# Kernel optimization log

Measured on AMD Instinct MI355X. Metric: run time of the kernel, lower is better.

Reference implementation:

```python
import jax, jax.numpy as jnp
import numpy as np

C = 192   # channels (class attr)
N = 196   # tokens per stream; 2N = 392, R feat dim = 784
B = 256

def _pw(x, w, b):
    # 1x1 Conv1d == pointwise channel mix: x [B,Ci,L] -> [B,Co,L]
    return jnp.einsum('oi,bil->bol', w, x) + b[None, :, None]

def _bn(x, g, beta, m, v):
    # eval-mode BatchNorm1d
    inv = g / jnp.sqrt(v + 1e-5)
    return (x - m[None, :, None]) * inv[None, :, None] + beta[None, :, None]

def setup_inputs():
    key = jax.random.key(0)
    ks = jax.random.split(key, 24)
    s = 1.0 / np.sqrt(C)
    d = {}
    d['x'] = jax.random.normal(ks[0], (B, N, C), dtype=jnp.float32)
    d['y'] = jax.random.normal(ks[1], (B, N, C), dtype=jnp.float32)
    # linear_conv_1: Conv1d(C,C,1) + BN + ReLU
    d['w1'] = jax.random.normal(ks[2], (C, C), dtype=jnp.float32) * s
    d['b1'] = jax.random.normal(ks[3], (C,), dtype=jnp.float32) * 0.01
    d['g1'] = jnp.ones((C,), jnp.float32)
    d['be1'] = jnp.zeros((C,), jnp.float32)
    d['m1'] = jax.random.normal(ks[4], (C,), dtype=jnp.float32) * 0.1
    d['v1'] = jax.random.uniform(ks[5], (C,), dtype=jnp.float32) + 0.5
    # linear_conv_2
    d['w2'] = jax.random.normal(ks[6], (C, C), dtype=jnp.float32) * s
    d['b2'] = jax.random.normal(ks[7], (C,), dtype=jnp.float32) * 0.01
    d['g2'] = jnp.ones((C,), jnp.float32)
    d['be2'] = jnp.zeros((C,), jnp.float32)
    d['m2'] = jax.random.normal(ks[8], (C,), dtype=jnp.float32) * 0.1
    d['v2'] = jax.random.uniform(ks[9], (C,), dtype=jnp.float32) + 0.5
    # linear_conv_3: Conv1d(C,C,1)
    d['w3'] = jax.random.normal(ks[10], (C, C), dtype=jnp.float32) * s
    d['b3'] = jax.random.normal(ks[11], (C,), dtype=jnp.float32) * 0.01
    # linear_conv_4: Conv1d(784,784,1)
    d['w4'] = jax.random.normal(ks[12], (784, 784), dtype=jnp.float32) / np.sqrt(784)
    d['b4'] = jax.random.normal(ks[13], (784,), dtype=jnp.float32) * 0.01
    # linear_conv_5: Conv1d(C+784,1,1)
    d['w5'] = jax.random.normal(ks[14], (1, C + 784), dtype=jnp.float32) / np.sqrt(C + 784)
    d['b5'] = jax.random.normal(ks[15], (1,), dtype=jnp.float32) * 0.01
    return d

def reference(x, y, w1, b1, g1, be1, m1, v1, w2, b2, g2, be2, m2, v2, w3, b3, w4, b4, w5, b5):
    xp = jnp.swapaxes(x, 1, 2)  # [B,C,N]
    yp = jnp.swapaxes(y, 1, 2)
    phi_x = jax.nn.relu(_bn(_pw(xp, w1, b1), g1, be1, m1, v1))
    phi_y = jax.nn.relu(_bn(_pw(yp, w2, b2), g2, be2, m2, v2))
    cat_phi = jnp.concatenate([phi_x, phi_y], axis=2)            # [B,C,2N]
    A = jnp.einsum('bcn,bcm->bnm', cat_phi, cat_phi)             # [B,2N,2N]
    # R[b,i,:] = cat(A[b,i,:], A[b,:,i]) for i in 0..2N-1, then permute(0,2,1)
    R = jnp.concatenate([A, jnp.swapaxes(A, 1, 2)], axis=2)      # [B,2N,4N]
    R = jnp.swapaxes(R, 1, 2)                                    # [B,4N,2N] = [B,784,392]
    v = _pw(cat_phi, w3, b3)                                     # [B,C,392]
    v_ = _pw(R, w4, b4)                                          # [B,784,392]
    cat_v = jnp.concatenate([v, v_], axis=1)                     # [B,976,392]
    W = _pw(cat_v, w5, b5)                                       # [B,1,392]
    out = xp * W[:, :, :N] + yp * W[:, :, N:]                    # [B,C,N]
    return out
```

## Files before the change

### kernel.cpp

```cpp
#include <hip/hip_runtime.h>
#include <hip/hip_bf16.h>

typedef __attribute__((ext_vector_type(8))) short bf16x8;
typedef __attribute__((ext_vector_type(4))) float f32x4;

#define CDIM 192
#define NTOK 196
#define LTOT 392
#define BDIM 256
#define NBE 64

__device__ __forceinline__ ushort f2bf(float f) {
  uint u = __float_as_uint(f);
  u = (u + 0x7FFFu + ((u >> 16) & 1u)) >> 16;
  return (ushort)u;
}
__device__ __forceinline__ float bf2f(ushort h) {
  return __uint_as_float(((uint)h) << 16);
}
__device__ __forceinline__ uint pk2(float lo, float hi) {
  __hip_bfloat162 t = __float22bfloat162_rn(float2{lo, hi});
  uint r;
  __builtin_memcpy(&r, &t, 4);
  return r;
}
__device__ __forceinline__ float wave_reduce(float a) {
#pragma unroll
  for (int off = 32; off > 0; off >>= 1) a += __shfl_xor(a, off);
  return a;
}

__global__ __launch_bounds__(256) void prep_kernel(
    const float* __restrict__ w1, const float* __restrict__ b1, const float* __restrict__ g1,
    const float* __restrict__ be1, const float* __restrict__ m1, const float* __restrict__ v1,
    const float* __restrict__ w2, const float* __restrict__ b2, const float* __restrict__ g2,
    const float* __restrict__ be2, const float* __restrict__ m2, const float* __restrict__ v2,
    const float* __restrict__ w3, const float* __restrict__ b3,
    const float* __restrict__ w4, const float* __restrict__ b4,
    const float* __restrict__ w5, const float* __restrict__ b5,
    ushort* __restrict__ w1b, ushort* __restrict__ w2b,
    float* __restrict__ u3, float* __restrict__ u4, float* __restrict__ cvecs,
    float* __restrict__ Kc, float* __restrict__ s) {
  const int bid = blockIdx.x;
  const int wid = threadIdx.x >> 6, lane = threadIdx.x & 63;
  if (bid < NBE) {
    for (int i = bid * BDIM + threadIdx.x; i < 123264; i += NBE * BDIM) {
      if (i < 36864) {
        int o = i / CDIM;
        float inv = g1[o] * rsqrtf(v1[o] + 1e-5f);
        w1b[i] = f2bf(w1[i] * inv);
      } else if (i < 73728) {
        int j = i - 36864; int o = j / CDIM;
        float inv = g2[o] * rsqrtf(v2[o] + 1e-5f);
        w2b[j] = f2bf(w2[j] * inv);
      } else if (i < 74112) {
        int k = i - 73728; int h = k / CDIM, o = k % CDIM;
        const float* bb = h ? b2 : b1; const float* gg = h ? g2 : g1;
        const float* bee = h ? be2 : be1;
        const float* mm = h ? m2 : m1; const float* vv = h ? v2 : v1;
        float inv = gg[o] * rsqrtf(vv[o] + 1e-5f);
        cvecs[k] = (bb[o] - mm[o]) * inv + bee[o];
      } else {
        s[i - 74112] = 0.f;
      }
    }
  } else if (bid < NBE + 48) {
    int j = (bid - NBE) * 4 + wid;
    float a = 0.f;
    for (int c = lane; c < CDIM; c += 64) a += w5[c] * w3[c * CDIM + j];
    a = wave_reduce(a);
    if (lane == 0) u3[j] = a;
  } else if (bid < NBE + 48 + 98) {
    int j = (bid - NBE - 48) * 4 + wid;
    float a = 0.f;
    for (int o = lane; o < 784; o += 64)
      a += w5[CDIM + o] * (w4[o * 784 + j] + w4[o * 784 + j + LTOT]);
    a = wave_reduce(a);
    if (lane == 0) u4[j] = a;
  } else {
    if (wid == 0) {
      float a = 0.f;
      for (int i = lane; i < CDIM + 784; i += 64)
        a += (i < CDIM) ? w5[i] * b3[i] : w5[i] * b4[i - CDIM];
      a = wave_reduce(a);
      if (lane == 0) Kc[0] = a + b5[0];
    }
  }
}

__global__ __launch_bounds__(256) void phi_kernel(
    const float* __restrict__ x, const float* __restrict__ y,
    const ushort* __restrict__ w1b, const ushort* __restrict__ w2b,
    const float* __restrict__ cvecs, const float* __restrict__ u4,
    ushort* __restrict__ phiT, float* __restrict__ s) {
  const int bh = blockIdx.x, b = bh >> 1, h = bh & 1;
  const float* __restrict__ src = (h ? y : x) + (size_t)b * NTOK * CDIM;
  const ushort* __restrict__ wb = h ? w2b : w1b;
  __shared__ ushort Abuf[2][32 * CDIM];
  __shared__ ushort Obuf[32 * CDIM];
  __shared__ float u4s[224];
  __shared__ float cs[CDIM];
  const int tid = threadIdx.x;
  for (int i = tid; i < 224; i += BDIM) u4s[i] = (i < NTOK) ? u4[h * NTOK + i] : 0.f;
  for (int i = tid; i < CDIM; i += BDIM) cs[i] = cvecs[h * CDIM + i];

  const int wid = tid >> 6, lane = tid & 63;
  const int lrow = lane & 15, kgrp = lane >> 4;
  const int cbase = wid * 48 + lrow;

  bf16x8 bfr[3][6];
#pragma unroll
  for (int ct = 0; ct < 3; ct++)
#pragma unroll
    for (int kk = 0; kk < 6; kk++)
      bfr[ct][kk] = *(const bf16x8*)(wb + (size_t)(cbase + ct * 16) * CDIM + kk * 32 + kgrp * 8);
  __syncthreads();
  const float csr[3] = {cs[cbase], cs[cbase + 16], cs[cbase + 32]};

  const float4* src4 = (const float4*)src;
  const int NF4 = NTOK * CDIM / 4;
  float sp[3] = {0.f, 0.f, 0.f};

  float4 pf[6];
#pragma unroll
  for (int p = 0; p < 6; p++) {
    pf[p] = src4[p * 256 + tid];
  }

  for (int r = 0; r < 7; r++) {
    ushort* Ab = &Abuf[r & 1][0];
#pragma unroll
    for (int p = 0; p < 6; p++) {
      const int fi = r * 1536 + p * 256 + tid;
      const int rowg = fi / 48;
      const int col = (fi - rowg * 48) * 4;
      const int rl = rowg & 31;
      uint2 wv;
      if (fi < NF4) { wv.x = pk2(pf[p].x, pf[p].y); wv.y = pk2(pf[p].z, pf[p].w); }
      else          { wv.x = 0u; wv.y = 0u; }
      uint addr = (uint)(rl * (CDIM * 2) + col * 2);
      addr ^= (uint)((rl & 7) << 4);
      *(uint2*)((char*)Ab + addr) = wv;
    }
    if (r < 6) {
#pragma unroll
      for (int p = 0; p < 6; p++) {
        const int fi = (r + 1) * 1536 + p * 256 + tid;
        pf[p] = (fi < NF4) ? src4[fi] : float4{0.f, 0.f, 0.f, 0.f};
      }
    }
    __syncthreads();
#pragma unroll
    for (int tt = 0; tt < 2; tt++) {
      bf16x8 afr[6];
#pragma unroll
      for (int kk = 0; kk < 6; kk++) {
        uint addr = (uint)((tt * 16 + lrow) * (CDIM * 2) + (kk * 32 + kgrp * 8) * 2);
        addr ^= (uint)((lrow & 7) << 4);
        afr[kk] = *(const bf16x8*)((const char*)Ab + addr);
      }
      f32x4 acc0 = {0.f,0.f,0.f,0.f}, acc1 = {0.f,0.f,0.f,0.f}, acc2 = {0.f,0.f,0.f,0.f};
#pragma unroll
      for (int kk = 0; kk < 6; kk++) {
        acc0 = __builtin_amdgcn_mfma_f32_16x16x32_bf16(afr[kk], bfr[0][kk], acc0, 0, 0, 0);
        acc1 = __builtin_amdgcn_mfma_f32_16x16x32_bf16(afr[kk], bfr[1][kk], acc1, 0, 0, 0);
        acc2 = __builtin_amdgcn_mfma_f32_16x16x32_bf16(afr[kk], bfr[2][kk], acc2, 0, 0, 0);
      }
      const int ll = tt * 16 + 4 * kgrp;
      const float4 u4v = *(const float4*)&u4s[r * 32 + ll];
      auto epi = [&](const f32x4& acc, int ct, float& spc) {
        const float v0 = fmaxf(acc[0] + csr[ct], 0.f);
        const float v1 = fmaxf(acc[1] + csr[ct], 0.f);
        const float v2 = fmaxf(acc[2] + csr[ct], 0.f);
        const float v3 = fmaxf(acc[3] + csr[ct], 0.f);
        const uint p01 = pk2(v0, v1), p23 = pk2(v2, v3);
        const int c = cbase + ct * 16;
#pragma unroll
        for (int j = 0; j < 4; j++) {
          const int row = ll + j;
          uint addr = (uint)(row * (CDIM * 2) + c * 2);
          addr ^= (uint)((row & 7) << 4);
          const uint piece = (j == 0) ? (p01 & 0xFFFFu) : (j == 1) ? (p01 >> 16)
                           : (j == 2) ? (p23 & 0xFFFFu) : (p23 >> 16);
          *(ushort*)((char*)Obuf + addr) = (ushort)piece;
        }
        spc += u4v.x * v0 + u4v.y * v1 + u4v.z * v2 + u4v.w * v3;
      };
      epi(acc0, 0, sp[0]); epi(acc1, 1, sp[1]); epi(acc2, 2, sp[2]);
    }
    __syncthreads();
    const int rows = min(32, NTOK - r * 32);
    const int nel = rows * CDIM;
    ushort* dst = phiT + ((size_t)b * LTOT + h * NTOK + r * 32) * CDIM;
    for (int off = tid * 8; off < nel; off += BDIM * 8) {
      const int row = off / CDIM;
      uint addr = (uint)(off * 2) ^ (uint)((row & 7) << 4);
      uint4 v = *(const uint4*)((const char*)Obuf + addr);
      *(uint4*)(dst + off) = v;
    }
  }
#pragma unroll
  for (int ct = 0; ct < 3; ct++) {
    float v = sp[ct];
    v += __shfl_xor(v, 16);
    v += __shfl_xor(v, 32);
    if (kgrp == 0) atomicAdd(&s[b * CDIM + cbase + ct * 16], v);
  }
}

__global__ __launch_bounds__(256) void wout_kernel(
    const float* __restrict__ x, const float* __restrict__ y,
    const ushort* __restrict__ phiT, const float* __restrict__ s,
    const float* __restrict__ u3, const float* __restrict__ Kc,
    float* __restrict__ out) {
  const int bid = blockIdx.x;
  const int b = bid / 7, nt = bid % 7;
  const int n0 = nt * 28;
  __shared__ float coeff[CDIM];
  __shared__ float Wl[56];
  __shared__ float tile[28][193];
  const int tid = threadIdx.x;
  for (int i = tid; i < CDIM; i += BDIM) coeff[i] = u3[i] + s[b * CDIM + i];
  __syncthreads();
  const int wv = tid >> 6, lane = tid & 63;
  const int rloc = wv * 16 + (lane >> 2), g4 = lane & 3;
  if (rloc < 56) {
    const int lg = (rloc < 28) ? (n0 + rloc) : (NTOK + n0 + rloc - 28);
    const ushort* p = phiT + ((size_t)b * LTOT + lg) * CDIM + g4 * 48;
    float acc = 0.f;
#pragma unroll
    for (int q = 0; q < 12; q++) {
      ushort4 v = *(const ushort4*)(p + q * 4);
      const float* cf = &coeff[g4 * 48 + q * 4];
      acc += cf[0] * bf2f(v.x) + cf[1] * bf2f(v.y) +
             cf[2] * bf2f(v.z) + cf[3] * bf2f(v.w);
    }
    acc += __shfl_xor(acc, 1);
    acc += __shfl_xor(acc, 2);
    if (g4 == 0) Wl[rloc] = acc + Kc[0];
  }
  __syncthreads();
  for (int i = tid; i < 28 * 48; i += BDIM) {
    const int nl = i / 48, c4 = (i % 48) * 4;
    const size_t xi = ((size_t)b * NTOK + n0 + nl) * CDIM + c4;
    const float4 xv = *(const float4*)&x[xi];
    const float4 yv = *(const float4*)&y[xi];
    const float wx = Wl[nl], wy = Wl[28 + nl];
    tile[nl][c4 + 0] = xv.x * wx + yv.x * wy;
    tile[nl][c4 + 1] = xv.y * wx + yv.y * wy;
    tile[nl][c4 + 2] = xv.z * wx + yv.z * wy;
    tile[nl][c4 + 3] = xv.w * wx + yv.w * wy;
  }
  __syncthreads();
  for (int i = tid; i < CDIM * 7; i += BDIM) {
    const int c = i / 7, nq = i % 7;
    float4 o;
    o.x = tile[nq * 4 + 0][c]; o.y = tile[nq * 4 + 1][c];
    o.z = tile[nq * 4 + 2][c]; o.w = tile[nq * 4 + 3][c];
    *(float4*)&out[((size_t)b * CDIM + c) * NTOK + n0 + nq * 4] = o;
  }
}

extern "C" void kernel_launch(void* const* d_in, const int* in_sizes, int n_in,
                              void* d_out, int out_size, void* d_ws, size_t ws_size,
                              hipStream_t stream) {
  const float* x   = (const float*)d_in[0];
  const float* y   = (const float*)d_in[1];
  const float* w1  = (const float*)d_in[2];
  const float* b1  = (const float*)d_in[3];
  const float* g1  = (const float*)d_in[4];
  const float* be1 = (const float*)d_in[5];
  const float* m1  = (const float*)d_in[6];
  const float* v1  = (const float*)d_in[7];
  const float* w2  = (const float*)d_in[8];
  const float* b2  = (const float*)d_in[9];
  const float* g2  = (const float*)d_in[10];
  const float* be2 = (const float*)d_in[11];
  const float* m2  = (const float*)d_in[12];
  const float* v2  = (const float*)d_in[13];
  const float* w3  = (const float*)d_in[14];
  const float* b3  = (const float*)d_in[15];
  const float* w4  = (const float*)d_in[16];
  const float* b4  = (const float*)d_in[17];
  const float* w5  = (const float*)d_in[18];
  const float* b5  = (const float*)d_in[19];
  float* out = (float*)d_out;

  char* ws = (char*)d_ws;
  ushort* w1b  = (ushort*)ws;
  ushort* w2b  = (ushort*)(ws + 73728);
  float* fbase = (float*)(ws + 147456);
  float* u3    = fbase;
  float* u4    = fbase + 192;
  float* cvecs = fbase + 584;
  float* Kc    = fbase + 968;
  float* s     = fbase + 976;
  ushort* phiT = (ushort*)(ws + (1 << 22));

  prep_kernel<<<211, BDIM, 0, stream>>>(w1, b1, g1, be1, m1, v1,
                                        w2, b2, g2, be2, m2, v2,
                                        w3, b3, w4, b4, w5, b5,
                                        w1b, w2b, u3, u4, cvecs, Kc, s);
  phi_kernel<<<512, BDIM, 0, stream>>>(x, y, w1b, w2b, cvecs, u4, phiT, s);
  wout_kernel<<<256 * 7, BDIM, 0, stream>>>(x, y, phiT, s, u3, Kc, out);
}
```

Measured before the change: 62.16 us.

## Fuse phi computation and W reduction per batch, keep phi in LDS

Replaces the per-(batch, stream) phi kernel with one 768-thread block per batch. The block keeps the full 392x192 bf16 phi matrix in shared memory, reduces s locally without global atomics, and computes the W vector in-block. This removes the phiT round trip through global memory and the atomics. The output kernel now only reads the precomputed W. In exchange, only 256 blocks run, each using about 155KB of LDS, so occupancy and parallelism are lower.

Measured after the change: 67.65 us. 8.8% more time.

```diff
diff --git a/kernel.cpp b/kernel.cpp
--- a/kernel.cpp
+++ b/kernel.cpp
@@ -7,7 +7,6 @@
 #define CDIM 192
 #define NTOK 196
 #define LTOT 392
-#define BDIM 256
 #define NBE 64
 
 __device__ __forceinline__ ushort f2bf(float f) {
@@ -40,11 +39,11 @@
     const float* __restrict__ w5, const float* __restrict__ b5,
     ushort* __restrict__ w1b, ushort* __restrict__ w2b,
     float* __restrict__ u3, float* __restrict__ u4, float* __restrict__ cvecs,
-    float* __restrict__ Kc, float* __restrict__ s) {
+    float* __restrict__ Kc) {
   const int bid = blockIdx.x;
   const int wid = threadIdx.x >> 6, lane = threadIdx.x & 63;
   if (bid < NBE) {
-    for (int i = bid * BDIM + threadIdx.x; i < 123264; i += NBE * BDIM) {
+    for (int i = bid * 256 + threadIdx.x; i < 74112; i += NBE * 256) {
       if (i < 36864) {
         int o = i / CDIM;
         float inv = g1[o] * rsqrtf(v1[o] + 1e-5f);
@@ -53,15 +52,13 @@
         int j = i - 36864; int o = j / CDIM;
         float inv = g2[o] * rsqrtf(v2[o] + 1e-5f);
         w2b[j] = f2bf(w2[j] * inv);
-      } else if (i < 74112) {
+      } else {
         int k = i - 73728; int h = k / CDIM, o = k % CDIM;
         const float* bb = h ? b2 : b1; const float* gg = h ? g2 : g1;
         const float* bee = h ? be2 : be1;
         const float* mm = h ? m2 : m1; const float* vv = h ? v2 : v1;
         float inv = gg[o] * rsqrtf(vv[o] + 1e-5f);
         cvecs[k] = (bb[o] - mm[o]) * inv + bee[o];
-      } else {
-        s[i - 74112] = 0.f;
       }
     }
   } else if (bid < NBE + 48) {
@@ -88,159 +85,180 @@
   }
 }
 
-__global__ __launch_bounds__(256) void phi_kernel(
+#define PHIL_BYTES (404 * 384)
+#define OFF_U4S PHIL_BYTES
+#define OFF_CSL (OFF_U4S + 1600)
+#define OFF_SARR (OFF_CSL + 1536)
+#define SMEM_BYTES (OFF_SARR + 768)
+
+extern __shared__ char smem[];
+
+__global__ __launch_bounds__(768, 1) void fused_kernel(
     const float* __restrict__ x, const float* __restrict__ y,
     const ushort* __restrict__ w1b, const ushort* __restrict__ w2b,
     const float* __restrict__ cvecs, const float* __restrict__ u4,
-    ushort* __restrict__ phiT, float* __restrict__ s) {
-  const int bh = blockIdx.x, b = bh >> 1, h = bh & 1;
-  const float* __restrict__ src = (h ? y : x) + (size_t)b * NTOK * CDIM;
-  const ushort* __restrict__ wb = h ? w2b : w1b;
-  __shared__ ushort Abuf[2][32 * CDIM];
-  __shared__ ushort Obuf[32 * CDIM];
-  __shared__ float u4s[224];
-  __shared__ float cs[CDIM];
+    const float* __restrict__ u3, const float* __restrict__ Kc,
+    float* __restrict__ Wg) {
+  const int b = blockIdx.x;
+  ushort* phiL = (ushort*)smem;
+  float* u4s = (float*)(smem + OFF_U4S);
+  float* csL = (float*)(smem + OFF_CSL);
+  float* sArr = (float*)(smem + OFF_SARR);
   const int tid = threadIdx.x;
-  for (int i = tid; i < 224; i += BDIM) u4s[i] = (i < NTOK) ? u4[h * NTOK + i] : 0.f;
-  for (int i = tid; i < CDIM; i += BDIM) cs[i] = cvecs[h * CDIM + i];
-
-  const int wid = tid >> 6, lane = tid & 63;
+  for (int i = tid; i < 400; i += 768) u4s[i] = (i < LTOT) ? u4[i] : 0.f;
+  for (int i = tid; i < 384; i += 768) csL[i] = cvecs[i];
+
+  const int w = tid >> 6, lane = tid & 63;
   const int lrow = lane & 15, kgrp = lane >> 4;
-  const int cbase = wid * 48 + lrow;
-
-  bf16x8 bfr[3][6];
-#pragma unroll
-  for (int ct = 0; ct < 3; ct++)
-#pragma unroll
-    for (int kk = 0; kk < 6; kk++)
-      bfr[ct][kk] = *(const bf16x8*)(wb + (size_t)(cbase + ct * 16) * CDIM + kk * 32 + kgrp * 8);
-  __syncthreads();
-  const float csr[3] = {cs[cbase], cs[cbase + 16], cs[cbase + 32]};
-
-  const float4* src4 = (const float4*)src;
-  const int NF4 = NTOK * CDIM / 4;
-  float sp[3] = {0.f, 0.f, 0.f};
-
-  float4 pf[6];
-#pragma unroll
-  for (int p = 0; p < 6; p++) {
-    pf[p] = src4[p * 256 + tid];
-  }
-
-  for (int r = 0; r < 7; r++) {
-    ushort* Ab = &Abuf[r & 1][0];
-#pragma unroll
-    for (int p = 0; p < 6; p++) {
-      const int fi = r * 1536 + p * 256 + tid;
-      const int rowg = fi / 48;
-      const int col = (fi - rowg * 48) * 4;
-      const int rl = rowg & 31;
-      uint2 wv;
-      if (fi < NF4) { wv.x = pk2(pf[p].x, pf[p].y); wv.y = pk2(pf[p].z, pf[p].w); }
-      else          { wv.x = 0u; wv.y = 0u; }
-      uint addr = (uint)(rl * (CDIM * 2) + col * 2);
-      addr ^= (uint)((rl & 7) << 4);
-      *(uint2*)((char*)Ab + addr) = wv;
-    }
-    if (r < 6) {
-#pragma unroll
-      for (int p = 0; p < 6; p++) {
-        const int fi = (r + 1) * 1536 + p * 256 + tid;
-        pf[p] = (fi < NF4) ? src4[fi] : float4{0.f, 0.f, 0.f, 0.f};
-      }
-    }
+  const int c = w * 16 + lrow;
+
+  bf16x8 bfr0[6], bfr1[6];
+#pragma unroll
+  for (int kk = 0; kk < 6; kk++) {
+    bfr0[kk] = *(const bf16x8*)(w1b + (size_t)c * CDIM + kk * 32 + kgrp * 8);
+    bfr1[kk] = *(const bf16x8*)(w2b + (size_t)c * CDIM + kk * 32 + kgrp * 8);
+  }
+  __syncthreads();
+  const float csr0 = csL[c], csr1 = csL[CDIM + c];
+
+  const float4* xb4 = (const float4*)(x + (size_t)b * NTOK * CDIM);
+  const float4* yb4 = (const float4*)(y + (size_t)b * NTOK * CDIM);
+  float sp = 0.f;
+
+  auto loadpf = [&](int R, float4* pf) {
+    if (R < 14) {
+      const float4* s4 = (R < 7) ? xb4 : yb4;
+      const int base = (R % 7) * 1536;
+#pragma unroll
+      for (int p = 0; p < 2; p++) {
+        const int fi = base + p * 768 + tid;
+        pf[p] = (fi < 9408) ? s4[fi] : float4{0.f, 0.f, 0.f, 0.f};
+      }
+    }
+  };
+  float4 pfA[2], pfB[2];
+  loadpf(0, pfA);
+  loadpf(1, pfB);
+
+  for (int R = 0; R < 14; R++) {
+    const int h = R / 7, r = R % 7;
+#pragma unroll
+    for (int p = 0; p < 2; p++) {
+      const int fi = r * 1536 + p * 768 + tid;
+      if (fi < 9408) {
+        const int row = fi / 48, c4 = fi - row * 48;
+        const int l = h * NTOK + row;
+        uint2 wv;
+        wv.x = pk2(pfA[p].x, pfA[p].y);
+        wv.y = pk2(pfA[p].z, pfA[p].w);
+        uint addr = (uint)(l * 384 + c4 * 8) ^ (uint)((l & 7) << 4);
+        *(uint2*)((char*)phiL + addr) = wv;
+      }
+    }
+    pfA[0] = pfB[0]; pfA[1] = pfB[1];
+    loadpf(R + 2, pfB);
     __syncthreads();
-#pragma unroll
-    for (int tt = 0; tt < 2; tt++) {
-      bf16x8 afr[6];
+
+    const bool t1ok = (r * 32 + 16) < NTOK;
+    f32x4 acc0 = {0.f, 0.f, 0.f, 0.f}, acc1 = {0.f, 0.f, 0.f, 0.f};
+    {
+      bf16x8 a0[6], a1[6];
+      const int l0 = h * NTOK + r * 32 + lrow;
 #pragma unroll
       for (int kk = 0; kk < 6; kk++) {
-        uint addr = (uint)((tt * 16 + lrow) * (CDIM * 2) + (kk * 32 + kgrp * 8) * 2);
-        addr ^= (uint)((lrow & 7) << 4);
-        afr[kk] = *(const bf16x8*)((const char*)Ab + addr);
-      }
-      f32x4 acc0 = {0.f,0.f,0.f,0.f}, acc1 = {0.f,0.f,0.f,0.f}, acc2 = {0.f,0.f,0.f,0.f};
-#pragma unroll
-      for (int kk = 0; kk < 6; kk++) {
-        acc0 = __builtin_amdgcn_mfma_f32_16x16x32_bf16(afr[kk], bfr[0][kk], acc0, 0, 0, 0);
-        acc1 = __builtin_amdgcn_mfma_f32_16x16x32_bf16(afr[kk], bfr[1][kk], acc1, 0, 0, 0);
-        acc2 = __builtin_amdgcn_mfma_f32_16x16x32_bf16(afr[kk], bfr[2][kk], acc2, 0, 0, 0);
-      }
-      const int ll = tt * 16 + 4 * kgrp;
-      const float4 u4v = *(const float4*)&u4s[r * 32 + ll];
-      auto epi = [&](const f32x4& acc, int ct, float& spc) {
-        const float v0 = fmaxf(acc[0] + csr[ct], 0.f);
-        const float v1 = fmaxf(acc[1] + csr[ct], 0.f);
-        const float v2 = fmaxf(acc[2] + csr[ct], 0.f);
-        const float v3 = fmaxf(acc[3] + csr[ct], 0.f);
-        const uint p01 = pk2(v0, v1), p23 = pk2(v2, v3);
-        const int c = cbase + ct * 16;
-#pragma unroll
-        for (int j = 0; j < 4; j++) {
-          const int row = ll + j;
-          uint addr = (uint)(row * (CDIM * 2) + c * 2);
-          addr ^= (uint)((row & 7) << 4);
-          const uint piece = (j == 0) ? (p01 & 0xFFFFu) : (j == 1) ? (p01 >> 16)
-                           : (j == 2) ? (p23 & 0xFFFFu) : (p23 >> 16);
-          *(ushort*)((char*)Obuf + addr) = (ushort)piece;
+        uint ad0 = (uint)(l0 * 384 + (kk * 32 + kgrp * 8) * 2) ^ (uint)((l0 & 7) << 4);
+        a0[kk] = *(const bf16x8*)((const char*)phiL + ad0);
+        const int l1 = l0 + 16;
+        uint ad1 = (uint)(l1 * 384 + (kk * 32 + kgrp * 8) * 2) ^ (uint)((l1 & 7) << 4);
+        a1[kk] = *(const bf16x8*)((const char*)phiL + ad1);
+      }
+      if (h == 0) {
+#pragma unroll
+        for (int kk = 0; kk < 6; kk++) {
+          acc0 = __builtin_amdgcn_mfma_f32_16x16x32_bf16(a0[kk], bfr0[kk], acc0, 0, 0, 0);
+          if (t1ok) acc1 = __builtin_amdgcn_mfma_f32_16x16x32_bf16(a1[kk], bfr0[kk], acc1, 0, 0, 0);
         }
-        spc += u4v.x * v0 + u4v.y * v1 + u4v.z * v2 + u4v.w * v3;
-      };
-      epi(acc0, 0, sp[0]); epi(acc1, 1, sp[1]); epi(acc2, 2, sp[2]);
+      } else {
+#pragma unroll
+        for (int kk = 0; kk < 6; kk++) {
+          acc0 = __builtin_amdgcn_mfma_f32_16x16x32_bf16(a0[kk], bfr1[kk], acc0, 0, 0, 0);
+          if (t1ok) acc1 = __builtin_amdgcn_mfma_f32_16x16x32_bf16(a1[kk], bfr1[kk], acc1, 0, 0, 0);
+        }
+      }
     }
     __syncthreads();
-    const int rows = min(32, NTOK - r * 32);
-    const int nel = rows * CDIM;
-    ushort* dst = phiT + ((size_t)b * LTOT + h * NTOK + r * 32) * CDIM;
-    for (int off = tid * 8; off < nel; off += BDIM * 8) {
-      const int row = off / CDIM;
-      uint addr = (uint)(off * 2) ^ (uint)((row & 7) << 4);
-      uint4 v = *(const uint4*)((const char*)Obuf + addr);
-      *(uint4*)(dst + off) = v;
-    }
-  }
-#pragma unroll
-  for (int ct = 0; ct < 3; ct++) {
-    float v = sp[ct];
-    v += __shfl_xor(v, 16);
-    v += __shfl_xor(v, 32);
-    if (kgrp == 0) atomicAdd(&s[b * CDIM + cbase + ct * 16], v);
-  }
-}
-
-__global__ __launch_bounds__(256) void wout_kernel(
+
+    {
+      const float csr = h ? csr1 : csr0;
+#pragma unroll
+      for (int tt = 0; tt < 2; tt++) {
+        const int rb = r * 32 + tt * 16;
+        if (rb < NTOK) {
+          const f32x4 ac = tt ? acc1 : acc0;
+          const float v0 = fmaxf(ac[0] + csr, 0.f);
+          const float v1 = fmaxf(ac[1] + csr, 0.f);
+          const float v2 = fmaxf(ac[2] + csr, 0.f);
+          const float v3 = fmaxf(ac[3] + csr, 0.f);
+          const uint p01 = pk2(v0, v1), p23 = pk2(v2, v3);
+          const int row0 = rb + 4 * kgrp;
+#pragma unroll
+          for (int j = 0; j < 4; j++) {
+            const int row = row0 + j;
+            if (row < NTOK) {
+              const int l = h * NTOK + row;
+              uint addr = (uint)(l * 384 + c * 2) ^ (uint)((l & 7) << 4);
+              const uint piece = (j == 0) ? (p01 & 0xFFFFu) : (j == 1) ? (p01 >> 16)
+                               : (j == 2) ? (p23 & 0xFFFFu) : (p23 >> 16);
+              *(ushort*)((char*)phiL + addr) = (ushort)piece;
+              const float vj = (j == 0) ? v0 : (j == 1) ? v1 : (j == 2) ? v2 : v3;
+              sp += u4s[l] * vj;
+            }
+          }
+        }
+      }
+    }
+  }
+
+  sp += __shfl_xor(sp, 16);
+  sp += __shfl_xor(sp, 32);
+  if (kgrp == 0) sArr[c] = sp;
+  __syncthreads();
+  for (int i = tid; i < CDIM; i += 768) sArr[i] = u3[i] + sArr[i];
+  __syncthreads();
+
+  const float Kv = Kc[0];
+  const int grp = tid >> 2, g4 = tid & 3;
+  for (int l = grp; l < LTOT; l += 192) {
+    float acc = 0.f;
+#pragma unroll
+    for (int q = 0; q < 12; q++) {
+      const int cc = g4 * 48 + q * 4;
+      uint addr = (uint)(l * 384 + cc * 2) ^ (uint)((l & 7) << 4);
+      ushort4 v = *(const ushort4*)((const char*)phiL + addr);
+      acc += sArr[cc] * bf2f(v.x) + sArr[cc + 1] * bf2f(v.y) +
+             sArr[cc + 2] * bf2f(v.z) + sArr[cc + 3] * bf2f(v.w);
+    }
+    acc += __shfl_xor(acc, 1);
+    acc += __shfl_xor(acc, 2);
+    if (g4 == 0) Wg[b * LTOT + l] = acc + Kv;
+  }
+}
+
+__global__ __launch_bounds__(256) void out_kernel(
     const float* __restrict__ x, const float* __restrict__ y,
-    const ushort* __restrict__ phiT, const float* __restrict__ s,
-    const float* __restrict__ u3, const float* __restrict__ Kc,
-    float* __restrict__ out) {
+    const float* __restrict__ Wg, float* __restrict__ out) {
   const int bid = blockIdx.x;
   const int b = bid / 7, nt = bid % 7;
   const int n0 = nt * 28;
-  __shared__ float coeff[CDIM];
   __shared__ float Wl[56];
   __shared__ float tile[28][193];
   const int tid = threadIdx.x;
-  for (int i = tid; i < CDIM; i += BDIM) coeff[i] = u3[i] + s[b * CDIM + i];
-  __syncthreads();
-  const int wv = tid >> 6, lane = tid & 63;
-  const int rloc = wv * 16 + (lane >> 2), g4 = lane & 3;
-  if (rloc < 56) {
-    const int lg = (rloc < 28) ? (n0 + rloc) : (NTOK + n0 + rloc - 28);
-    const ushort* p = phiT + ((size_t)b * LTOT + lg) * CDIM + g4 * 48;
-    float acc = 0.f;
-#pragma unroll
-    for (int q = 0; q < 12; q++) {
-      ushort4 v = *(const ushort4*)(p + q * 4);
-      const float* cf = &coeff[g4 * 48 + q * 4];
-      acc += cf[0] * bf2f(v.x) + cf[1] * bf2f(v.y) +
-             cf[2] * bf2f(v.z) + cf[3] * bf2f(v.w);
-    }
-    acc += __shfl_xor(acc, 1);
-    acc += __shfl_xor(acc, 2);
-    if (g4 == 0) Wl[rloc] = acc + Kc[0];
-  }
-  __syncthreads();
-  for (int i = tid; i < 28 * 48; i += BDIM) {
+  if (tid < 56) {
+    const int lg = (tid < 28) ? (n0 + tid) : (NTOK + n0 + tid - 28);
+    Wl[tid] = Wg[b * LTOT + lg];
+  }
+  __syncthreads();
+  for (int i = tid; i < 28 * 48; i += 256) {
     const int nl = i / 48, c4 = (i % 48) * 4;
     const size_t xi = ((size_t)b * NTOK + n0 + nl) * CDIM + c4;
     const float4 xv = *(const float4*)&x[xi];
@@ -252,7 +270,7 @@
     tile[nl][c4 + 3] = xv.w * wx + yv.w * wy;
   }
   __syncthreads();
-  for (int i = tid; i < CDIM * 7; i += BDIM) {
+  for (int i = tid; i < CDIM * 7; i += 256) {
     const int c = i / 7, nq = i % 7;
     float4 o;
     o.x = tile[nq * 4 + 0][c]; o.y = tile[nq * 4 + 1][c];
@@ -294,13 +312,13 @@
   float* u4    = fbase + 192;
   float* cvecs = fbase + 584;
   float* Kc    = fbase + 968;
-  float* s     = fbase + 976;
-  ushort* phiT = (ushort*)(ws + (1 << 22));
-
-  prep_kernel<<<211, BDIM, 0, stream>>>(w1, b1, g1, be1, m1, v1,
-                                        w2, b2, g2, be2, m2, v2,
-                                        w3, b3, w4, b4, w5, b5,
-                                        w1b, w2b, u3, u4, cvecs, Kc, s);
-  phi_kernel<<<512, BDIM, 0, stream>>>(x, y, w1b, w2b, cvecs, u4, phiT, s);
-  wout_kernel<<<256 * 7, BDIM, 0, stream>>>(x, y, phiT, s, u3, Kc, out);
-}
+  float* Wg    = fbase + 976;
+
+  prep_kernel<<<211, 256, 0, stream>>>(w1, b1, g1, be1, m1, v1,
+                                       w2, b2, g2, be2, m2, v2,
+                                       w3, b3, w4, b4, w5, b5,
+                                       w1b, w2b, u3, u4, cvecs, Kc);
+  fused_kernel<<<256, 768, SMEM_BYTES, stream>>>(x, y, w1b, w2b, cvecs, u4,
+                                                 u3, Kc, Wg);
+  out_kernel<<<256 * 7, 256, 0, stream>>>(x, y, Wg, out);
+}
```

## Stream phi inputs via global_load_lds into swizzled fp32 LDS double buffer

Applied to the files above, without the earlier changes.

The register-staged prefetch of x/y tiles (load float4, convert to bf16, store to LDS) is replaced by direct global-to-LDS 16-byte loads into an XOR-swizzled fp32 double buffer, with explicit vmcnt waits and raw barriers. Conversion to bf16 now happens when MFMA A fragments are read from LDS. Partial tail tiles are skipped and the u4 reduction is masked per row, and MFMA sections get raised scheduling priority. This frees registers and VALU work in the load path but doubles LDS footprint for the input buffers and adds conversion work on the read side.

New measurement: 70.38 us. +13.2%, slower.

```diff
diff --git a/kernel.cpp b/kernel.cpp
--- a/kernel.cpp
+++ b/kernel.cpp
@@ -28,6 +28,16 @@
 #pragma unroll
   for (int off = 32; off > 0; off >>= 1) a += __shfl_xor(a, off);
   return a;
+}
+__device__ __forceinline__ void barL() {
+  asm volatile("s_waitcnt lgkmcnt(0)" ::: "memory");
+  __builtin_amdgcn_s_barrier();
+  __builtin_amdgcn_sched_barrier(0);
+}
+__device__ __forceinline__ void gload16(const void* g, void* l) {
+  __builtin_amdgcn_global_load_lds(
+      (const __attribute__((address_space(1))) void*)g,
+      (__attribute__((address_space(3))) void*)l, 16, 0, 0);
 }
 
 __global__ __launch_bounds__(256) void prep_kernel(
@@ -96,7 +106,7 @@
   const int bh = blockIdx.x, b = bh >> 1, h = bh & 1;
   const float* __restrict__ src = (h ? y : x) + (size_t)b * NTOK * CDIM;
   const ushort* __restrict__ wb = h ? w2b : w1b;
-  __shared__ ushort Abuf[2][32 * CDIM];
+  __shared__ float Af[2][32 * CDIM];
   __shared__ ushort Obuf[32 * CDIM];
   __shared__ float u4s[224];
   __shared__ float cs[CDIM];
@@ -117,78 +127,83 @@
   __syncthreads();
   const float csr[3] = {cs[cbase], cs[cbase + 16], cs[cbase + 32]};
 
-  const float4* src4 = (const float4*)src;
-  const int NF4 = NTOK * CDIM / 4;
+  auto issue = [&](int r) {
+    const int row0 = r * 32;
+#pragma unroll
+    for (int j = 0; j < 6; j++) {
+      const int slot = wid * 6 + j;
+      const int lin = slot * 1024 + lane * 16;
+      const int row = lin / 768;
+      const int oin = lin - row * 768;
+      const int srow = min(row0 + row, NTOK - 1);
+      const int goff = srow * 768 + (oin ^ ((row & 15) << 4));
+      gload16((const char*)src + goff, (char*)&Af[r & 1][0] + slot * 1024);
+    }
+  };
+  issue(0);
+
   float sp[3] = {0.f, 0.f, 0.f};
-
-  float4 pf[6];
-#pragma unroll
-  for (int p = 0; p < 6; p++) {
-    pf[p] = src4[p * 256 + tid];
-  }
-
   for (int r = 0; r < 7; r++) {
-    ushort* Ab = &Abuf[r & 1][0];
-#pragma unroll
-    for (int p = 0; p < 6; p++) {
-      const int fi = r * 1536 + p * 256 + tid;
-      const int rowg = fi / 48;
-      const int col = (fi - rowg * 48) * 4;
-      const int rl = rowg & 31;
-      uint2 wv;
-      if (fi < NF4) { wv.x = pk2(pf[p].x, pf[p].y); wv.y = pk2(pf[p].z, pf[p].w); }
-      else          { wv.x = 0u; wv.y = 0u; }
-      uint addr = (uint)(rl * (CDIM * 2) + col * 2);
-      addr ^= (uint)((rl & 7) << 4);
-      *(uint2*)((char*)Ab + addr) = wv;
-    }
     if (r < 6) {
-#pragma unroll
-      for (int p = 0; p < 6; p++) {
-        const int fi = (r + 1) * 1536 + p * 256 + tid;
-        pf[p] = (fi < NF4) ? src4[fi] : float4{0.f, 0.f, 0.f, 0.f};
+      issue(r + 1);
+      asm volatile("s_waitcnt vmcnt(6)" ::: "memory");
+    } else {
+      asm volatile("s_waitcnt vmcnt(0)" ::: "memory");
+    }
+    __builtin_amdgcn_sched_barrier(0);
+    barL();
+    const char* Ab = (const char*)&Af[r & 1][0];
+#pragma unroll
+    for (int tt = 0; tt < 2; tt++) {
+      const int l0 = r * 32 + tt * 16;
+      if (l0 < NTOK) {
+        bf16x8 afr[6];
+#pragma unroll
+        for (int kk = 0; kk < 6; kk++) {
+          const int row = tt * 16 + lrow;
+          const uint m = (uint)((row & 15) << 4);
+          const uint colb = (uint)((kk * 32 + kgrp * 8) * 4);
+          const f32x4 f0 = *(const f32x4*)(Ab + row * 768 + (int)(colb ^ m));
+          const f32x4 f1 = *(const f32x4*)(Ab + row * 768 + (int)((colb + 16) ^ m));
+          uint4 au;
+          au.x = pk2(f0[0], f0[1]); au.y = pk2(f0[2], f0[3]);
+          au.z = pk2(f1[0], f1[1]); au.w = pk2(f1[2], f1[3]);
+          __builtin_memcpy(&afr[kk], &au, 16);
+        }
+        f32x4 acc0 = {0.f,0.f,0.f,0.f}, acc1 = {0.f,0.f,0.f,0.f}, acc2 = {0.f,0.f,0.f,0.f};
+        __builtin_amdgcn_s_setprio(1);
+#pragma unroll
+        for (int kk = 0; kk < 6; kk++) {
+          acc0 = __builtin_amdgcn_mfma_f32_16x16x32_bf16(afr[kk], bfr[0][kk], acc0, 0, 0, 0);
+          acc1 = __builtin_amdgcn_mfma_f32_16x16x32_bf16(afr[kk], bfr[1][kk], acc1, 0, 0, 0);
+          acc2 = __builtin_amdgcn_mfma_f32_16x16x32_bf16(afr[kk], bfr[2][kk], acc2, 0, 0, 0);
+        }
+        __builtin_amdgcn_s_setprio(0);
+        const int ll = tt * 16 + 4 * kgrp;
+        const float4 u4v = *(const float4*)&u4s[r * 32 + ll];
+        auto epi = [&](const f32x4& acc, int ct, float& spc) {
+          const float v0 = fmaxf(acc[0] + csr[ct], 0.f);
+          const float v1 = fmaxf(acc[1] + csr[ct], 0.f);
+          const float v2 = fmaxf(acc[2] + csr[ct], 0.f);
+          const float v3 = fmaxf(acc[3] + csr[ct], 0.f);
+          const uint p01 = pk2(v0, v1), p23 = pk2(v2, v3);
+          const int c = cbase + ct * 16;
+#pragma unroll
+          for (int j = 0; j < 4; j++) {
+            const int row = ll + j;
+            uint addr = (uint)(row * (CDIM * 2) + c * 2);
+            addr ^= (uint)((row & 7) << 4);
+            const uint piece = (j == 0) ? (p01 & 0xFFFFu) : (j == 1) ? (p01 >> 16)
+                             : (j == 2) ? (p23 & 0xFFFFu) : (p23 >> 16);
+            *(ushort*)((char*)Obuf + addr) = (ushort)piece;
+            const float vj = (j == 0) ? v0 : (j == 1) ? v1 : (j == 2) ? v2 : v3;
+            if (l0 - tt * 16 + row < NTOK) spc += u4v.x * 0.f + u4s[r * 32 + row] * vj;
+          }
+        };
+        epi(acc0, 0, sp[0]); epi(acc1, 1, sp[1]); epi(acc2, 2, sp[2]);
       }
     }
-    __syncthreads();
-#pragma unroll
-    for (int tt = 0; tt < 2; tt++) {
-      bf16x8 afr[6];
-#pragma unroll
-      for (int kk = 0; kk < 6; kk++) {
-        uint addr = (uint)((tt * 16 + lrow) * (CDIM * 2) + (kk * 32 + kgrp * 8) * 2);
-        addr ^= (uint)((lrow & 7) << 4);
-        afr[kk] = *(const bf16x8*)((const char*)Ab + addr);
-      }
-      f32x4 acc0 = {0.f,0.f,0.f,0.f}, acc1 = {0.f,0.f,0.f,0.f}, acc2 = {0.f,0.f,0.f,0.f};
-#pragma unroll
-      for (int kk = 0; kk < 6; kk++) {
-        acc0 = __builtin_amdgcn_mfma_f32_16x16x32_bf16(afr[kk], bfr[0][kk], acc0, 0, 0, 0);
-        acc1 = __builtin_amdgcn_mfma_f32_16x16x32_bf16(afr[kk], bfr[1][kk], acc1, 0, 0, 0);
-        acc2 = __builtin_amdgcn_mfma_f32_16x16x32_bf16(afr[kk], bfr[2][kk], acc2, 0, 0, 0);
-      }
-      const int ll = tt * 16 + 4 * kgrp;
-      const float4 u4v = *(const float4*)&u4s[r * 32 + ll];
-      auto epi = [&](const f32x4& acc, int ct, float& spc) {
-        const float v0 = fmaxf(acc[0] + csr[ct], 0.f);
-        const float v1 = fmaxf(acc[1] + csr[ct], 0.f);
-        const float v2 = fmaxf(acc[2] + csr[ct], 0.f);
-        const float v3 = fmaxf(acc[3] + csr[ct], 0.f);
-        const uint p01 = pk2(v0, v1), p23 = pk2(v2, v3);
-        const int c = cbase + ct * 16;
-#pragma unroll
-        for (int j = 0; j < 4; j++) {
-          const int row = ll + j;
-          uint addr = (uint)(row * (CDIM * 2) + c * 2);
-          addr ^= (uint)((row & 7) << 4);
-          const uint piece = (j == 0) ? (p01 & 0xFFFFu) : (j == 1) ? (p01 >> 16)
-                           : (j == 2) ? (p23 & 0xFFFFu) : (p23 >> 16);
-          *(ushort*)((char*)Obuf + addr) = (ushort)piece;
-        }
-        spc += u4v.x * v0 + u4v.y * v1 + u4v.z * v2 + u4v.w * v3;
-      };
-      epi(acc0, 0, sp[0]); epi(acc1, 1, sp[1]); epi(acc2, 2, sp[2]);
-    }
-    __syncthreads();
+    barL();
     const int rows = min(32, NTOK - r * 32);
     const int nel = rows * CDIM;
     ushort* dst = phiT + ((size_t)b * LTOT + h * NTOK + r * 32) * CDIM;
```
